# Performance work log

Hardware: AMD Instinct MI355X
Metric: run time of the kernel (lower is better)

## Reference

```python
import jax, jax.numpy as jnp
import numpy as np

B, H, W, C, NH, WS, NB = 8, 64, 64, 384, 12, 8, 2
N = H * W
NWT = WS * WS  # tokens per window
SHIFT = WS // 2

def _rel_index(ws):
    coords = np.stack(np.meshgrid(np.arange(ws), np.arange(ws), indexing='ij')).reshape(2, -1)
    rel = (coords[:, :, None] - coords[:, None, :]).transpose(1, 2, 0)
    rel[..., 0] += ws - 1
    rel[..., 1] += ws - 1
    rel[..., 0] *= 2 * ws - 1
    return rel.sum(-1)  # (ws*ws, ws*ws)

REL_IDX = _rel_index(WS)

def _shift_mask(h, w, ws, shift):
    img = np.zeros((h, w))
    cnt = 0
    for hs in (slice(0, -ws), slice(-ws, -shift), slice(-shift, None)):
        for wsl in (slice(0, -ws), slice(-ws, -shift), slice(-shift, None)):
            img[hs, wsl] = cnt
            cnt += 1
    win = img.reshape(h // ws, ws, w // ws, ws).transpose(0, 2, 1, 3).reshape(-1, ws * ws)
    diff = win[:, None, :] - win[:, :, None]
    return np.where(diff != 0, -100.0, 0.0).astype(np.float32)  # (nW, NWT, NWT)

MASK = jnp.asarray(_shift_mask(H, W, WS, SHIFT))

def _ln(x, g, b, eps=1e-5):
    m = jnp.mean(x, -1, keepdims=True)
    v = jnp.mean((x - m) ** 2, -1, keepdims=True)
    return (x - m) * jax.lax.rsqrt(v + eps) * g + b

def _partition(x):
    b = x.shape[0]
    x = x.reshape(b, H // WS, WS, W // WS, WS, C).transpose(0, 1, 3, 2, 4, 5)
    return x.reshape(-1, NWT, C)

def _reverse(wx, b):
    x = wx.reshape(b, H // WS, W // WS, WS, WS, C).transpose(0, 1, 3, 2, 4, 5)
    return x.reshape(b, H, W, C)

def _attention(xw, qkv_w, qkv_b, proj_w, proj_b, rpb, mask):
    B_, Nt, Cc = xw.shape
    hd = Cc // NH
    qkv = (xw @ qkv_w + qkv_b).reshape(B_, Nt, 3, NH, hd).transpose(2, 0, 3, 1, 4)
    q, k, v = qkv[0], qkv[1], qkv[2]
    bias = rpb[REL_IDX].transpose(2, 0, 1)[None]  # (1, NH, Nt, Nt)
    attn = jnp.einsum('bhnd,bhmd->bhnm', q * (hd ** -0.5), k) + bias
    if mask is not None:
        nW = mask.shape[0]
        attn = attn.reshape(B_ // nW, nW, NH, Nt, Nt) + mask[None, :, None]
        attn = attn.reshape(B_, NH, Nt, Nt)
    attn = jax.nn.softmax(attn, axis=-1)
    out = jnp.einsum('bhnm,bhmd->bhnd', attn, v).transpose(0, 2, 1, 3).reshape(B_, Nt, Cc)
    return out @ proj_w + proj_b

def _swin_block(x, p, shift):
    n1g, n1b, n2g, n2b, qw, qb, pw, pb, w1, b1, w2, b2, rpb = p
    shortcut = x
    h = _ln(x, n1g, n1b)
    if shift > 0:
        h = jnp.roll(h, (-shift, -shift), axis=(1, 2))
    hw = _attention(_partition(h), qw, qb, pw, pb, rpb, MASK if shift > 0 else None)
    h = _reverse(hw, x.shape[0])
    if shift > 0:
        h = jnp.roll(h, (shift, shift), axis=(1, 2))
    x = shortcut + h
    h = _ln(x, n2g, n2b)
    h = jax.nn.gelu(h @ w1 + b1) @ w2 + b2
    return x + h


def setup_inputs() -> dict:
    key = jax.random.key(0)
    ks = jax.random.split(key, 6)
    s = 0.02
    return {
        'x': jax.random.normal(ks[0], (B, N, C), jnp.float32),
        'outer_g': jnp.ones((NB, C), jnp.float32),
        'outer_b': jnp.zeros((NB, C), jnp.float32),
        'n1_g': jnp.ones((NB, C), jnp.float32),
        'n1_b': jnp.zeros((NB, C), jnp.float32),
        'n2_g': jnp.ones((NB, C), jnp.float32),
        'n2_b': jnp.zeros((NB, C), jnp.float32),
        'qkv_w': jax.random.normal(ks[1], (NB, C, 3 * C), jnp.float32) * s,
        'qkv_b': jnp.zeros((NB, 3 * C), jnp.float32),
        'proj_w': jax.random.normal(ks[2], (NB, C, C), jnp.float32) * s,
        'proj_b': jnp.zeros((NB, C), jnp.float32),
        'mlp_w1': jax.random.normal(ks[3], (NB, C, 4 * C), jnp.float32) * s,
        'mlp_b1': jnp.zeros((NB, 4 * C), jnp.float32),
        'mlp_w2': jax.random.normal(ks[4], (NB, 4 * C, C), jnp.float32) * s,
        'mlp_b2': jnp.zeros((NB, C), jnp.float32),
        'rpb': jax.random.normal(ks[5], (NB, (2 * WS - 1) ** 2, NH), jnp.float32) * s,
    }


def reference(x, outer_g, outer_b, n1_g, n1_b, n2_g, n2_b, qkv_w, qkv_b, proj_w, proj_b, mlp_w1, mlp_b1, mlp_w2, mlp_b2, rpb):
    xv = x.reshape(B, H, W, C)
    for i in range(NB):
        shift = 0 if i % 2 == 0 else SHIFT
        p = (n1_g[i], n1_b[i], n2_g[i], n2_b[i], qkv_w[i], qkv_b[i], proj_w[i], proj_b[i],
             mlp_w1[i], mlp_b1[i], mlp_w2[i], mlp_b2[i], rpb[i])
        residual = xv
        xv = _swin_block(_ln(xv, outer_g[i], outer_b[i]), p, shift) + residual
    return xv.reshape(B, N, C)
```

## Files before the change

kernel.cpp:

```cpp
#include <hip/hip_runtime.h>
#include <hip/hip_bf16.h>

#define BATCH 8
#define HDIM 64
#define WDIM 64
#define CC 384
#define NHE 12
#define HD 32
#define NTOK 32768
#define NBLK 2

typedef short short8 __attribute__((ext_vector_type(8)));
typedef float f32x4 __attribute__((ext_vector_type(4)));

__device__ __forceinline__ float bf2f(unsigned short u) {
  return __uint_as_float(((unsigned int)u) << 16);
}
__device__ __forceinline__ unsigned short f2bf(float f) {
  __hip_bfloat16 h = __float2bfloat16(f);
  return *reinterpret_cast<unsigned short*>(&h);
}
__device__ __forceinline__ float wave_sum(float s) {
#pragma unroll
  for (int o = 32; o; o >>= 1) s += __shfl_xor(s, o, 64);
  return s;
}
__device__ __forceinline__ float gelu_f(float x) {
  float y = 0.7978845608028654f * (x + 0.044715f * x * x * x);
  float t = 1.0f - 2.0f / (__expf(2.0f * y) + 1.0f);
  return 0.5f * x * (1.0f + t);
}
__device__ __forceinline__ int regid(int x) {
  return x < 56 ? 0 : (x < 60 ? 1 : 2);
}
__device__ __forceinline__ void gload16(const void* g, void* l) {
  __builtin_amdgcn_global_load_lds(
      (const __attribute__((address_space(1))) unsigned int*)g,
      (__attribute__((address_space(3))) unsigned int*)l, 16, 0, 0);
}

__global__ __launch_bounds__(256) void wconv_kernel(
    const float* __restrict__ src, unsigned short* __restrict__ dst, int K, int N) {
  __shared__ float tile[64 * 65];
  const int bn = blockIdx.x * 64, bk = blockIdx.y * 64;
  const int t = threadIdx.x;
  const int lk = t >> 2, ln = (t & 3) * 16;
  const float* ps = src + (size_t)(bk + lk) * N + bn + ln;
#pragma unroll
  for (int j = 0; j < 4; ++j)
    *(float4*)&tile[lk * 65 + ln + 4 * j] = *(const float4*)(ps + 4 * j);
  __syncthreads();
  const int on = t >> 2, ok = (t & 3) * 16;
  unsigned short ob[16];
#pragma unroll
  for (int j = 0; j < 16; ++j) ob[j] = f2bf(tile[(ok + j) * 65 + on]);
  uint4* pd = (uint4*)(dst + (size_t)(bn + on) * K + bk + ok);
  pd[0] = ((const uint4*)ob)[0];
  pd[1] = ((const uint4*)ob)[1];
}

__global__ __launch_bounds__(256) void bias_prep_kernel(
    const float* __restrict__ rpb, float* __restrict__ biasT) {
  int idx = blockIdx.x * 256 + threadIdx.x;
  int m = idx & 63;
  int n = (idx >> 6) & 63;
  int h = idx >> 12;
  int dr = (n >> 3) - (m >> 3) + 7;
  int dc = (n & 7) - (m & 7) + 7;
  biasT[idx] = rpb[(dr * 15 + dc) * NHE + h];
}

__global__ __launch_bounds__(256) void ln_fused_kernel(
    const float* __restrict__ xin, const float* __restrict__ og,
    const float* __restrict__ ob, const float* __restrict__ n1g,
    const float* __restrict__ n1b, unsigned short* __restrict__ y0h,
    unsigned short* __restrict__ abuf, int shift) {
  const int lane = threadIdx.x & 63;
  const int token = blockIdx.x * 4 + (threadIdx.x >> 6);
  const float* px = xin + (size_t)token * CC;
  float v[6];
#pragma unroll
  for (int j = 0; j < 6; ++j) v[j] = px[j * 64 + lane];
  float s = 0.f;
#pragma unroll
  for (int j = 0; j < 6; ++j) s += v[j];
  s = wave_sum(s);
  float mean = s * (1.0f / CC);
  float q = 0.f;
#pragma unroll
  for (int j = 0; j < 6; ++j) { float d = v[j] - mean; q += d * d; }
  q = wave_sum(q);
  float rstd = rsqrtf(q * (1.0f / CC) + 1e-5f);
  unsigned short* py = y0h + (size_t)token * CC;
#pragma unroll
  for (int j = 0; j < 6; ++j) {
    int d = j * 64 + lane;
    float y = (v[j] - mean) * rstd * og[d] + ob[d];
    py[d] = f2bf(y);
    v[j] = y;
  }
  s = 0.f;
#pragma unroll
  for (int j = 0; j < 6; ++j) s += v[j];
  s = wave_sum(s);
  float mean2 = s * (1.0f / CC);
  q = 0.f;
#pragma unroll
  for (int j = 0; j < 6; ++j) { float d = v[j] - mean2; q += d * d; }
  q = wave_sum(q);
  float rstd2 = rsqrtf(q * (1.0f / CC) + 1e-5f);
  int b = token >> 12;
  int hh = (token >> 6) & 63;
  int ww = token & 63;
  int r = (hh - shift) & 63;
  int c = (ww - shift) & 63;
  int wrow = (((b << 6) + ((r >> 3) << 3) + (c >> 3)) << 6) + ((r & 7) << 3) + (c & 7);
  unsigned short* pa = abuf + (size_t)wrow * CC;
#pragma unroll
  for (int j = 0; j < 6; ++j) {
    int d = j * 64 + lane;
    pa[d] = f2bf((v[j] - mean2) * rstd2 * n1g[d] + n1b[d]);
  }
}

__global__ __launch_bounds__(256, 1) void apl_kernel(
    const unsigned short* __restrict__ qkv, const float* __restrict__ biasT,
    const unsigned short* __restrict__ y0h, const unsigned short* __restrict__ Btp,
    const float* __restrict__ pb, const float* __restrict__ g2,
    const float* __restrict__ b2, unsigned short* __restrict__ x1h,
    unsigned short* __restrict__ abuf, int shift) {
  __shared__ __align__(1024) char smem[65536];
  const int tid = threadIdx.x;
  const int wv = tid >> 6;
  const int lane = tid & 63;
  const int l0 = lane & 15;
  const int q = lane >> 4;
  const int wi = blockIdx.x;
  const int use_mask = (shift != 0);

  unsigned short* P16 = (unsigned short*)(smem + wv * 12288);
  unsigned short* Vt16 = (unsigned short*)(smem + wv * 12288 + 8192);
  float* Ol = (float*)(smem + wv * 12288);
  unsigned short* Obuf = (unsigned short*)(smem + 49152);

  f32x4 pacc[4][6] = {};

  for (int p = 0; p < 3; ++p) {
    const int h = 4 * p + wv;
    const unsigned short* qbase = qkv + (size_t)(wi * 64) * 1152 + h * HD;
    short8 kf[4], qf[4];
#pragma unroll
    for (int mt = 0; mt < 4; ++mt)
      kf[mt] = *(const short8*)(qbase + (size_t)(16 * mt + l0) * 1152 + CC + 8 * q);
#pragma unroll
    for (int nt = 0; nt < 4; ++nt)
      qf[nt] = *(const short8*)(qbase + (size_t)(16 * nt + l0) * 1152 + 8 * q);

    f32x4 acc[4][4];
    const float* bh = biasT + h * 4096;
#pragma unroll
    for (int mt = 0; mt < 4; ++mt)
#pragma unroll
      for (int nt = 0; nt < 4; ++nt)
        acc[mt][nt] = *(const f32x4*)(bh + (l0 + 16 * nt) * 64 + 16 * mt + 4 * q);

    {
      unsigned short varr[32];
      const uint4* pv = (const uint4*)(qbase + (size_t)lane * 1152 + 2 * CC);
      uint4* t4 = (uint4*)varr;
      t4[0] = pv[0]; t4[1] = pv[1]; t4[2] = pv[2]; t4[3] = pv[3];
#pragma unroll
      for (int d = 0; d < 32; ++d)
        Vt16[d * 64 + 8 * ((lane >> 3) ^ (d & 7)) + (lane & 7)] = varr[d];
    }

#pragma unroll
    for (int mt = 0; mt < 4; ++mt)
#pragma unroll
      for (int nt = 0; nt < 4; ++nt)
        acc[mt][nt] = __builtin_amdgcn_mfma_f32_16x16x32_bf16(kf[mt], qf[nt], acc[mt][nt], 0, 0, 0);

    if (use_mask) {
      int wloc = wi & 63;
      int wy = (wloc >> 3) * 8, wx = (wloc & 7) * 8;
      int idn[4], idm[16];
#pragma unroll
      for (int nt = 0; nt < 4; ++nt) {
        int n = l0 + 16 * nt;
        idn[nt] = regid(wy + (n >> 3)) * 3 + regid(wx + (n & 7));
      }
#pragma unroll
      for (int mt = 0; mt < 4; ++mt)
#pragma unroll
        for (int r = 0; r < 4; ++r) {
          int m = 16 * mt + 4 * q + r;
          idm[mt * 4 + r] = regid(wy + (m >> 3)) * 3 + regid(wx + (m & 7));
        }
#pragma unroll
      for (int mt = 0; mt < 4; ++mt)
#pragma unroll
        for (int nt = 0; nt < 4; ++nt)
#pragma unroll
          for (int r = 0; r < 4; ++r)
            acc[mt][nt][r] += (idm[mt * 4 + r] == idn[nt]) ? 0.0f : -100.0f;
    }

    float inv[4];
#pragma unroll
    for (int nt = 0; nt < 4; ++nt) {
      float m0 = -1e30f;
#pragma unroll
      for (int mt = 0; mt < 4; ++mt)
#pragma unroll
        for (int r = 0; r < 4; ++r) m0 = fmaxf(m0, acc[mt][nt][r]);
      m0 = fmaxf(m0, __shfl_xor(m0, 16, 64));
      m0 = fmaxf(m0, __shfl_xor(m0, 32, 64));
      float s0 = 0.f;
#pragma unroll
      for (int mt = 0; mt < 4; ++mt)
#pragma unroll
        for (int r = 0; r < 4; ++r) {
          float e = __expf(acc[mt][nt][r] - m0);
          acc[mt][nt][r] = e;
          s0 += e;
        }
      s0 += __shfl_xor(s0, 16, 64);
      s0 += __shfl_xor(s0, 32, 64);
      inv[nt] = 1.0f / s0;
    }

#pragma unroll
    for (int mt = 0; mt < 4; ++mt)
#pragma unroll
      for (int nt = 0; nt < 4; ++nt) {
        unsigned int lo = (unsigned int)f2bf(acc[mt][nt][0] * inv[nt]) |
                          ((unsigned int)f2bf(acc[mt][nt][1] * inv[nt]) << 16);
        unsigned int hi = (unsigned int)f2bf(acc[mt][nt][2] * inv[nt]) |
                          ((unsigned int)f2bf(acc[mt][nt][3] * inv[nt]) << 16);
        unsigned int* dst = (unsigned int*)&P16[(l0 + 16 * nt) * 64 +
                                                8 * ((2 * mt + (q >> 1)) ^ (l0 & 7)) + 4 * (q & 1)];
        dst[0] = lo;
        dst[1] = hi;
      }
    __syncthreads();

    f32x4 oacc[4][2] = {};
#pragma unroll
    for (int kt = 0; kt < 2; ++kt) {
      short8 pa[4], vb[2];
#pragma unroll
      for (int nt = 0; nt < 4; ++nt)
        pa[nt] = *(const short8*)&P16[(l0 + 16 * nt) * 64 + 8 * ((q + 4 * kt) ^ (l0 & 7))];
#pragma unroll
      for (int dt = 0; dt < 2; ++dt)
        vb[dt] = *(const short8*)&Vt16[(l0 + 16 * dt) * 64 + 8 * ((q + 4 * kt) ^ (l0 & 7))];
#pragma unroll
      for (int nt = 0; nt < 4; ++nt)
#pragma unroll
        for (int dt = 0; dt < 2; ++dt)
          oacc[nt][dt] = __builtin_amdgcn_mfma_f32_16x16x32_bf16(pa[nt], vb[dt], oacc[nt][dt], 0, 0, 0);
    }
    __syncthreads();

#pragma unroll
    for (int nt = 0; nt < 4; ++nt)
#pragma unroll
      for (int dt = 0; dt < 2; ++dt)
#pragma unroll
        for (int r = 0; r < 4; ++r)
          Ol[(16 * nt + 4 * q + r) * 34 + l0 + 16 * dt] = oacc[nt][dt][r];
    __syncthreads();

#pragma unroll
    for (int jj = 0; jj < 4; ++jj) {
      int c = 4 * wv + jj;
      int pos = (c & 8) | ((c ^ lane) & 7);
      unsigned short tmp[8];
#pragma unroll
      for (int e = 0; e < 8; ++e) tmp[e] = f2bf(Ol[lane * 34 + jj * 8 + e]);
      *(uint4*)&Obuf[lane * 128 + pos * 8] = *(const uint4*)tmp;
    }
    __syncthreads();

#pragma unroll
    for (int kfl = 0; kfl < 4; ++kfl) {
      short8 a[4], b[6];
      int c2 = kfl * 4 + q;
      int pos2 = (c2 & 8) | ((c2 ^ l0) & 7);
#pragma unroll
      for (int mt = 0; mt < 4; ++mt)
        a[mt] = *(const short8*)&Obuf[(16 * mt + l0) * 128 + pos2 * 8];
#pragma unroll
      for (int nt = 0; nt < 6; ++nt)
        b[nt] = *(const short8*)(Btp + (size_t)(wv * 96 + nt * 16 + l0) * 384 +
                                 128 * p + 32 * kfl + 8 * q);
#pragma unroll
      for (int mt = 0; mt < 4; ++mt)
#pragma unroll
        for (int nt = 0; nt < 6; ++nt)
          pacc[mt][nt] = __builtin_amdgcn_mfma_f32_16x16x32_bf16(a[mt], b[nt], pacc[mt][nt], 0, 0, 0);
    }
    __syncthreads();
  }

  float pbv[6], g2v[6], b2v[6];
#pragma unroll
  for (int nt = 0; nt < 6; ++nt) {
    int col = wv * 96 + nt * 16 + l0;
    pbv[nt] = pb[col];
    g2v[nt] = g2[col];
    b2v[nt] = b2[col];
  }
  int dstrow[4][4];
#pragma unroll
  for (int mt = 0; mt < 4; ++mt)
#pragma unroll
    for (int rr = 0; rr < 4; ++rr) {
      int m = 16 * mt + 4 * q + rr;
      int grow = wi * 64 + m;
      int b_ = grow >> 12;
      int wl = (grow >> 6) & 63;
      int t = grow & 63;
      int rs = ((wl >> 3) << 3) + (t >> 3);
      int cs = ((wl & 7) << 3) + (t & 7);
      int hh = (rs + shift) & 63;
      int ww = (cs + shift) & 63;
      dstrow[mt][rr] = (((b_ << 6) + hh) << 6) + ww;
    }
#pragma unroll
  for (int mt = 0; mt < 4; ++mt)
#pragma unroll
    for (int nt = 0; nt < 6; ++nt)
#pragma unroll
      for (int rr = 0; rr < 4; ++rr) {
        size_t dst = (size_t)dstrow[mt][rr] * CC + wv * 96 + nt * 16 + l0;
        pacc[mt][nt][rr] += pbv[nt] + bf2f(y0h[dst]);
      }
  float* part = (float*)(smem + 49152);
  float* stats = (float*)(smem + 49152 + 2048);
#pragma unroll
  for (int mt = 0; mt < 4; ++mt)
#pragma unroll
    for (int rr = 0; rr < 4; ++rr) {
      float s = 0.f, ss = 0.f;
#pragma unroll
      for (int nt = 0; nt < 6; ++nt) {
        float v = pacc[mt][nt][rr];
        s += v;
        ss += v * v;
      }
#pragma unroll
      for (int o = 8; o; o >>= 1) {
        s += __shfl_xor(s, o, 64);
        ss += __shfl_xor(ss, o, 64);
      }
      if (l0 == 0) {
        int m = 16 * mt + 4 * q + rr;
        part[(m * 4 + wv) * 2] = s;
        part[(m * 4 + wv) * 2 + 1] = ss;
      }
    }
  __syncthreads();
  if (tid < 64) {
    float s = 0.f, ss = 0.f;
#pragma unroll
    for (int w = 0; w < 4; ++w) {
      s += part[(tid * 4 + w) * 2];
      ss += part[(tid * 4 + w) * 2 + 1];
    }
    float mean = s * (1.0f / CC);
    float var = ss * (1.0f / CC) - mean * mean;
    stats[tid * 2] = mean;
    stats[tid * 2 + 1] = rsqrtf(var + 1e-5f);
  }
  __syncthreads();
#pragma unroll
  for (int mt = 0; mt < 4; ++mt)
#pragma unroll
    for (int rr = 0; rr < 4; ++rr) {
      int m = 16 * mt + 4 * q + rr;
      float mean = stats[m * 2];
      float rstd = stats[m * 2 + 1];
#pragma unroll
      for (int nt = 0; nt < 6; ++nt) {
        float v = pacc[mt][nt][rr];
        size_t dst = (size_t)dstrow[mt][rr] * CC + wv * 96 + nt * 16 + l0;
        x1h[dst] = f2bf(v);
        abuf[dst] = f2bf((v - mean) * rstd * g2v[nt] + b2v[nt]);
      }
    }
}

template <int EPI, int NN, int KK>
__global__ __launch_bounds__(256, 2) void gemm_kernel(
    const unsigned short* __restrict__ A, const unsigned short* __restrict__ Bt,
    const float* __restrict__ bias, float* __restrict__ outf,
    unsigned short* __restrict__ outb, const unsigned short* __restrict__ add0h,
    const float* __restrict__ add1f) {
  __shared__ __align__(1024) char smem[32768];
  unsigned short* As = (unsigned short*)smem;
  unsigned short* Bs = (unsigned short*)(smem + 16384);
  const int tid = threadIdx.x;
  const int lane = tid & 63;
  const int wv = tid >> 6;
  const int wm = wv & 1, wn = wv >> 1;
  const int rowBase = blockIdx.y * 128;
  const int colBase = blockIdx.x * 128;
  const int srow = lane >> 3;
  const int schunk = (lane & 7) ^ srow;
  const unsigned short* pA = A + (size_t)(rowBase + srow) * KK + 8 * schunk;
  const unsigned short* pB = Bt + (size_t)(colBase + srow) * KK + 8 * schunk;
  const int l0 = lane & 15;
  const int q = lane >> 4;
  f32x4 acc[4][4] = {};

  for (int k0 = 0; k0 < KK; k0 += 64) {
    __syncthreads();
#pragma unroll
    for (int i = 0; i < 4; ++i) {
      int c = i * 4 + wv;
      gload16(pA + (size_t)(8 * c) * KK + k0, (char*)As + c * 1024);
      gload16(pB + (size_t)(8 * c) * KK + k0, (char*)Bs + c * 1024);
    }
    __syncthreads();
#pragma unroll
    for (int ksub = 0; ksub < 2; ++ksub) {
      const int sc = ksub * 4 + q;
      short8 af[4], bfr[4];
#pragma unroll
      for (int im = 0; im < 4; ++im) {
        int r = wm * 64 + im * 16 + l0;
        af[im] = *(const short8*)&As[r * 64 + 8 * (sc ^ (r & 7))];
      }
#pragma unroll
      for (int in_ = 0; in_ < 4; ++in_) {
        int r = wn * 64 + in_ * 16 + l0;
        bfr[in_] = *(const short8*)&Bs[r * 64 + 8 * (sc ^ (r & 7))];
      }
#pragma unroll
      for (int im = 0; im < 4; ++im)
#pragma unroll
        for (int in_ = 0; in_ < 4; ++in_)
          acc[im][in_] = __builtin_amdgcn_mfma_f32_16x16x32_bf16(
              af[im], bfr[in_], acc[im][in_], 0, 0, 0);
    }
  }
  const int quad = lane >> 4;
  const int lc = lane & 15;
#pragma unroll
  for (int im = 0; im < 4; ++im) {
    int rb = rowBase + wm * 64 + im * 16 + quad * 4;
#pragma unroll
    for (int in_ = 0; in_ < 4; ++in_) {
      int gcol = colBase + wn * 64 + in_ * 16 + lc;
      float bv = bias[gcol];
#pragma unroll
      for (int r = 0; r < 4; ++r) {
        int grow = rb + r;
        float v = acc[im][in_][r] + bv;
        if (EPI == 0) {
          if (gcol < CC) v *= 0.17677669529663687f;
          outb[(size_t)grow * NN + gcol] = f2bf(v);
        } else if (EPI == 1) {
          outb[(size_t)grow * NN + gcol] = f2bf(gelu_f(v));
        } else {
          size_t dst = (size_t)grow * CC + gcol;
          outf[dst] = bf2f(add0h[dst]) + add1f[dst] + v;
        }
      }
    }
  }
}

extern "C" void kernel_launch(void* const* d_in, const int* in_sizes, int n_in,
                              void* d_out, int out_size, void* d_ws, size_t ws_size,
                              hipStream_t stream) {
  const float* x    = (const float*)d_in[0];
  const float* og   = (const float*)d_in[1];
  const float* ob   = (const float*)d_in[2];
  const float* n1g  = (const float*)d_in[3];
  const float* n1b  = (const float*)d_in[4];
  const float* n2g  = (const float*)d_in[5];
  const float* n2b  = (const float*)d_in[6];
  const float* qkvw = (const float*)d_in[7];
  const float* qkvb = (const float*)d_in[8];
  const float* pw   = (const float*)d_in[9];
  const float* pb   = (const float*)d_in[10];
  const float* w1   = (const float*)d_in[11];
  const float* b1   = (const float*)d_in[12];
  const float* w2   = (const float*)d_in[13];
  const float* b2   = (const float*)d_in[14];
  const float* rpb  = (const float*)d_in[15];
  float* out = (float*)d_out;

  char* ws = (char*)d_ws;
  unsigned short* y0h   = (unsigned short*)(ws);
  unsigned short* x1h   = (unsigned short*)(ws + 25165824);
  unsigned short* a_bf  = (unsigned short*)(ws + 50331648);
  unsigned short* big_bf= (unsigned short*)(ws + 100663296);
  unsigned short* wt    = (unsigned short*)(ws + 201326592);
  float* biasT          = (float*)(ws + 100663296 + 75497472);

  for (int i = 0; i < NBLK; ++i) {
    unsigned short* wq = wt + (size_t)i * 1769472;
    wconv_kernel<<<dim3(18, 6), 256, 0, stream>>>(qkvw + (size_t)i * 442368, wq, 384, 1152);
    wconv_kernel<<<dim3(6, 6), 256, 0, stream>>>(pw + (size_t)i * 147456, wq + 442368, 384, 384);
    wconv_kernel<<<dim3(24, 6), 256, 0, stream>>>(w1 + (size_t)i * 589824, wq + 589824, 384, 1536);
    wconv_kernel<<<dim3(6, 24), 256, 0, stream>>>(w2 + (size_t)i * 589824, wq + 1179648, 1536, 384);
  }

  for (int i = 0; i < NBLK; ++i) {
    const float* xin = (i == 0) ? x : out;
    int shift = (i & 1) ? 4 : 0;
    unsigned short* wq = wt + (size_t)i * 1769472;
    ln_fused_kernel<<<8192, 256, 0, stream>>>(xin, og + i * 384, ob + i * 384,
                                              n1g + i * 384, n1b + i * 384, y0h, a_bf, shift);
    gemm_kernel<0, 1152, 384><<<dim3(9, 256), 256, 0, stream>>>(
        a_bf, wq, qkvb + i * 1152, nullptr, big_bf, nullptr, nullptr);
    bias_prep_kernel<<<192, 256, 0, stream>>>(rpb + i * 2700, biasT);
    apl_kernel<<<512, 256, 0, stream>>>(big_bf, biasT, y0h, wq + 442368,
                                        pb + i * 384, n2g + i * 384, n2b + i * 384,
                                        x1h, a_bf, shift);
    gemm_kernel<1, 1536, 384><<<dim3(12, 256), 256, 0, stream>>>(
        a_bf, wq + 589824, b1 + i * 1536, nullptr, big_bf, nullptr, nullptr);
    gemm_kernel<3, 384, 1536><<<dim3(3, 256), 256, 0, stream>>>(
        big_bf, wq + 1179648, b2 + i * 384, out, nullptr, x1h, xin);
  }
}
```

Before: 708.6 us.

## Prefetch next head's QKV in attention kernel and relax block barriers

Loads the next head's K/Q/V fragments into registers while the current head is processed, which hides global load latency. Most block-wide __syncthreads calls are replaced with per-wave LDS waitcnt fences, since each wave owns its own P/V/O scratch region. MFMA sections are wrapped in s_setprio, and launch bounds are raised to 2 blocks per CU. The extra prefetch registers may raise register pressure, and the higher occupancy target could cause spills. The 64KB of shared memory per block may also stop a second block from fitting on a CU.

```diff
diff --git a/kernel.cpp b/kernel.cpp
--- a/kernel.cpp
+++ b/kernel.cpp
@@ -123,7 +123,7 @@
   }
 }
 
-__global__ __launch_bounds__(256, 1) void apl_kernel(
+__global__ __launch_bounds__(256, 2) void apl_kernel(
     const unsigned short* __restrict__ qkv, const float* __restrict__ biasT,
     const unsigned short* __restrict__ y0h, const unsigned short* __restrict__ Btp,
     const float* __restrict__ pb, const float* __restrict__ g2,
@@ -144,17 +144,34 @@
   unsigned short* Obuf = (unsigned short*)(smem + 49152);
 
   f32x4 pacc[4][6] = {};
-
+  const unsigned short* qkw = qkv + (size_t)(wi * 64) * 1152;
+
+#define LOADP(PP, KD, QD, VD)                                                        \
+  {                                                                                  \
+    const unsigned short* qb_ = qkw + (4 * (PP) + wv) * HD;                          \
+    const uint4* pv_ = (const uint4*)(qb_ + (size_t)lane * 1152 + 2 * CC);           \
+    VD[0] = pv_[0]; VD[1] = pv_[1]; VD[2] = pv_[2]; VD[3] = pv_[3];                  \
+    _Pragma("unroll") for (int mt_ = 0; mt_ < 4; ++mt_)                              \
+        KD[mt_] = *(const short8*)(qb_ + (size_t)(16 * mt_ + l0) * 1152 + CC + 8 * q); \
+    _Pragma("unroll") for (int nt_ = 0; nt_ < 4; ++nt_)                              \
+        QD[nt_] = *(const short8*)(qb_ + (size_t)(16 * nt_ + l0) * 1152 + 8 * q);    \
+  }
+#define LDS_FENCE() asm volatile("s_waitcnt lgkmcnt(0)" ::: "memory")
+
+  short8 kf[4], qf[4];
+  uint4 varr4[4];
+  LOADP(0, kf, qf, varr4);
+
+#pragma unroll
   for (int p = 0; p < 3; ++p) {
     const int h = 4 * p + wv;
-    const unsigned short* qbase = qkv + (size_t)(wi * 64) * 1152 + h * HD;
-    short8 kf[4], qf[4];
-#pragma unroll
-    for (int mt = 0; mt < 4; ++mt)
-      kf[mt] = *(const short8*)(qbase + (size_t)(16 * mt + l0) * 1152 + CC + 8 * q);
-#pragma unroll
-    for (int nt = 0; nt < 4; ++nt)
-      qf[nt] = *(const short8*)(qbase + (size_t)(16 * nt + l0) * 1152 + 8 * q);
+
+    {
+      const unsigned short* varr = (const unsigned short*)varr4;
+#pragma unroll
+      for (int d = 0; d < 32; ++d)
+        Vt16[d * 64 + 8 * ((lane >> 3) ^ (d & 7)) + (lane & 7)] = varr[d];
+    }
 
     f32x4 acc[4][4];
     const float* bh = biasT + h * 4096;
@@ -164,21 +181,17 @@
       for (int nt = 0; nt < 4; ++nt)
         acc[mt][nt] = *(const f32x4*)(bh + (l0 + 16 * nt) * 64 + 16 * mt + 4 * q);
 
-    {
-      unsigned short varr[32];
-      const uint4* pv = (const uint4*)(qbase + (size_t)lane * 1152 + 2 * CC);
-      uint4* t4 = (uint4*)varr;
-      t4[0] = pv[0]; t4[1] = pv[1]; t4[2] = pv[2]; t4[3] = pv[3];
-#pragma unroll
-      for (int d = 0; d < 32; ++d)
-        Vt16[d * 64 + 8 * ((lane >> 3) ^ (d & 7)) + (lane & 7)] = varr[d];
-    }
-
+    short8 kfn[4], qfn[4];
+    uint4 varrn[4];
+    if (p < 2) { LOADP(p + 1, kfn, qfn, varrn); }
+
+    __builtin_amdgcn_s_setprio(1);
 #pragma unroll
     for (int mt = 0; mt < 4; ++mt)
 #pragma unroll
       for (int nt = 0; nt < 4; ++nt)
         acc[mt][nt] = __builtin_amdgcn_mfma_f32_16x16x32_bf16(kf[mt], qf[nt], acc[mt][nt], 0, 0, 0);
+    __builtin_amdgcn_s_setprio(0);
 
     if (use_mask) {
       int wloc = wi & 63;
@@ -242,9 +255,10 @@
         dst[0] = lo;
         dst[1] = hi;
       }
-    __syncthreads();
+    LDS_FENCE();
 
     f32x4 oacc[4][2] = {};
+    __builtin_amdgcn_s_setprio(1);
 #pragma unroll
     for (int kt = 0; kt < 2; ++kt) {
       short8 pa[4], vb[2];
@@ -260,7 +274,8 @@
         for (int dt = 0; dt < 2; ++dt)
           oacc[nt][dt] = __builtin_amdgcn_mfma_f32_16x16x32_bf16(pa[nt], vb[dt], oacc[nt][dt], 0, 0, 0);
     }
-    __syncthreads();
+    __builtin_amdgcn_s_setprio(0);
+    LDS_FENCE();
 
 #pragma unroll
     for (int nt = 0; nt < 4; ++nt)
@@ -269,17 +284,23 @@
 #pragma unroll
         for (int r = 0; r < 4; ++r)
           Ol[(16 * nt + 4 * q + r) * 34 + l0 + 16 * dt] = oacc[nt][dt][r];
-    __syncthreads();
-
+    LDS_FENCE();
+
+    uint4 opack[4];
+    int posv[4];
 #pragma unroll
     for (int jj = 0; jj < 4; ++jj) {
       int c = 4 * wv + jj;
-      int pos = (c & 8) | ((c ^ lane) & 7);
+      posv[jj] = (c & 8) | ((c ^ lane) & 7);
       unsigned short tmp[8];
 #pragma unroll
       for (int e = 0; e < 8; ++e) tmp[e] = f2bf(Ol[lane * 34 + jj * 8 + e]);
-      *(uint4*)&Obuf[lane * 128 + pos * 8] = *(const uint4*)tmp;
-    }
+      opack[jj] = *(const uint4*)tmp;
+    }
+    __syncthreads();
+#pragma unroll
+    for (int jj = 0; jj < 4; ++jj)
+      *(uint4*)&Obuf[lane * 128 + posv[jj] * 8] = opack[jj];
     __syncthreads();
 
 #pragma unroll
@@ -294,14 +315,25 @@
       for (int nt = 0; nt < 6; ++nt)
         b[nt] = *(const short8*)(Btp + (size_t)(wv * 96 + nt * 16 + l0) * 384 +
                                  128 * p + 32 * kfl + 8 * q);
+      __builtin_amdgcn_s_setprio(1);
 #pragma unroll
       for (int mt = 0; mt < 4; ++mt)
 #pragma unroll
         for (int nt = 0; nt < 6; ++nt)
           pacc[mt][nt] = __builtin_amdgcn_mfma_f32_16x16x32_bf16(a[mt], b[nt], pacc[mt][nt], 0, 0, 0);
-    }
-    __syncthreads();
-  }
+      __builtin_amdgcn_s_setprio(0);
+    }
+
+    if (p < 2) {
+#pragma unroll
+      for (int j = 0; j < 4; ++j) {
+        kf[j] = kfn[j];
+        qf[j] = qfn[j];
+        varr4[j] = varrn[j];
+      }
+    }
+  }
+  __syncthreads();
 
   float pbv[6], g2v[6], b2v[6];
 #pragma unroll
@@ -389,6 +421,8 @@
         abuf[dst] = f2bf((v - mean) * rstd * g2v[nt] + b2v[nt]);
       }
     }
+#undef LOADP
+#undef LDS_FENCE
 }
 
 template <int EPI, int NN, int KK>
```

Result: no change. 702.2 us (-0.9%).

## Double-buffer GEMM LDS loads, relax attention barriers, and raise MFMA priority

Applied to the files above, without the earlier changes.

The GEMM kernel now prefetches the next K tile into a second LDS buffer, with vmcnt waits and raw barriers, so global loads overlap the MFMA work on the current tile. LDS use doubles to 64KB, which may limit occupancy under launch_bounds(256,2). In the attention kernel, block-wide __syncthreads on per-wave private LDS regions are replaced with lgkmcnt fences, leaving only the barriers around the shared Obuf. s_setprio is raised around MFMA sections to favour compute issue.

```diff
diff --git a/kernel.cpp b/kernel.cpp
--- a/kernel.cpp
+++ b/kernel.cpp
@@ -143,6 +143,8 @@
   float* Ol = (float*)(smem + wv * 12288);
   unsigned short* Obuf = (unsigned short*)(smem + 49152);
 
+#define LDS_FENCE() asm volatile("s_waitcnt lgkmcnt(0)" ::: "memory")
+
   f32x4 pacc[4][6] = {};
 
   for (int p = 0; p < 3; ++p) {
@@ -174,11 +176,13 @@
         Vt16[d * 64 + 8 * ((lane >> 3) ^ (d & 7)) + (lane & 7)] = varr[d];
     }
 
+    __builtin_amdgcn_s_setprio(1);
 #pragma unroll
     for (int mt = 0; mt < 4; ++mt)
 #pragma unroll
       for (int nt = 0; nt < 4; ++nt)
         acc[mt][nt] = __builtin_amdgcn_mfma_f32_16x16x32_bf16(kf[mt], qf[nt], acc[mt][nt], 0, 0, 0);
+    __builtin_amdgcn_s_setprio(0);
 
     if (use_mask) {
       int wloc = wi & 63;
@@ -242,9 +246,10 @@
         dst[0] = lo;
         dst[1] = hi;
       }
-    __syncthreads();
+    LDS_FENCE();
 
     f32x4 oacc[4][2] = {};
+    __builtin_amdgcn_s_setprio(1);
 #pragma unroll
     for (int kt = 0; kt < 2; ++kt) {
       short8 pa[4], vb[2];
@@ -260,7 +265,8 @@
         for (int dt = 0; dt < 2; ++dt)
           oacc[nt][dt] = __builtin_amdgcn_mfma_f32_16x16x32_bf16(pa[nt], vb[dt], oacc[nt][dt], 0, 0, 0);
     }
-    __syncthreads();
+    __builtin_amdgcn_s_setprio(0);
+    LDS_FENCE();
 
 #pragma unroll
     for (int nt = 0; nt < 4; ++nt)
@@ -269,17 +275,23 @@
 #pragma unroll
         for (int r = 0; r < 4; ++r)
           Ol[(16 * nt + 4 * q + r) * 34 + l0 + 16 * dt] = oacc[nt][dt][r];
-    __syncthreads();
-
+    LDS_FENCE();
+
+    uint4 opack[4];
+    int posv[4];
 #pragma unroll
     for (int jj = 0; jj < 4; ++jj) {
       int c = 4 * wv + jj;
-      int pos = (c & 8) | ((c ^ lane) & 7);
+      posv[jj] = (c & 8) | ((c ^ lane) & 7);
       unsigned short tmp[8];
 #pragma unroll
       for (int e = 0; e < 8; ++e) tmp[e] = f2bf(Ol[lane * 34 + jj * 8 + e]);
-      *(uint4*)&Obuf[lane * 128 + pos * 8] = *(const uint4*)tmp;
-    }
+      opack[jj] = *(const uint4*)tmp;
+    }
+    __syncthreads();
+#pragma unroll
+    for (int jj = 0; jj < 4; ++jj)
+      *(uint4*)&Obuf[lane * 128 + posv[jj] * 8] = opack[jj];
     __syncthreads();
 
 #pragma unroll
@@ -294,14 +306,16 @@
       for (int nt = 0; nt < 6; ++nt)
         b[nt] = *(const short8*)(Btp + (size_t)(wv * 96 + nt * 16 + l0) * 384 +
                                  128 * p + 32 * kfl + 8 * q);
+      __builtin_amdgcn_s_setprio(1);
 #pragma unroll
       for (int mt = 0; mt < 4; ++mt)
 #pragma unroll
         for (int nt = 0; nt < 6; ++nt)
           pacc[mt][nt] = __builtin_amdgcn_mfma_f32_16x16x32_bf16(a[mt], b[nt], pacc[mt][nt], 0, 0, 0);
-    }
-    __syncthreads();
-  }
+      __builtin_amdgcn_s_setprio(0);
+    }
+  }
+  __syncthreads();
 
   float pbv[6], g2v[6], b2v[6];
 #pragma unroll
@@ -389,6 +403,7 @@
         abuf[dst] = f2bf((v - mean) * rstd * g2v[nt] + b2v[nt]);
       }
     }
+#undef LDS_FENCE
 }
 
 template <int EPI, int NN, int KK>
@@ -397,9 +412,7 @@
     const float* __restrict__ bias, float* __restrict__ outf,
     unsigned short* __restrict__ outb, const unsigned short* __restrict__ add0h,
     const float* __restrict__ add1f) {
-  __shared__ __align__(1024) char smem[32768];
-  unsigned short* As = (unsigned short*)smem;
-  unsigned short* Bs = (unsigned short*)(smem + 16384);
+  __shared__ __align__(1024) char smem[65536];
   const int tid = threadIdx.x;
   const int lane = tid & 63;
   const int wv = tid >> 6;
@@ -414,15 +427,32 @@
   const int q = lane >> 4;
   f32x4 acc[4][4] = {};
 
+#pragma unroll
+  for (int i = 0; i < 4; ++i) {
+    int c = i * 4 + wv;
+    gload16(pA + (size_t)(8 * c) * KK, smem + c * 1024);
+    gload16(pB + (size_t)(8 * c) * KK, smem + 16384 + c * 1024);
+  }
+
+#pragma unroll 2
   for (int k0 = 0; k0 < KK; k0 += 64) {
-    __syncthreads();
-#pragma unroll
-    for (int i = 0; i < 4; ++i) {
-      int c = i * 4 + wv;
-      gload16(pA + (size_t)(8 * c) * KK + k0, (char*)As + c * 1024);
-      gload16(pB + (size_t)(8 * c) * KK + k0, (char*)Bs + c * 1024);
-    }
-    __syncthreads();
+    const int cur = (k0 >> 6) & 1;
+    char* curb = smem + cur * 32768;
+    if (k0 + 64 < KK) {
+      char* nxtb = smem + (cur ^ 1) * 32768;
+#pragma unroll
+      for (int i = 0; i < 4; ++i) {
+        int c = i * 4 + wv;
+        gload16(pA + (size_t)(8 * c) * KK + k0 + 64, nxtb + c * 1024);
+        gload16(pB + (size_t)(8 * c) * KK + k0 + 64, nxtb + 16384 + c * 1024);
+      }
+      asm volatile("s_waitcnt vmcnt(8)" ::: "memory");
+    } else {
+      asm volatile("s_waitcnt vmcnt(0)" ::: "memory");
+    }
+    __builtin_amdgcn_s_barrier();
+    const unsigned short* As = (const unsigned short*)curb;
+    const unsigned short* Bs = (const unsigned short*)(curb + 16384);
 #pragma unroll
     for (int ksub = 0; ksub < 2; ++ksub) {
       const int sc = ksub * 4 + q;
@@ -437,13 +467,16 @@
         int r = wn * 64 + in_ * 16 + l0;
         bfr[in_] = *(const short8*)&Bs[r * 64 + 8 * (sc ^ (r & 7))];
       }
+      __builtin_amdgcn_s_setprio(1);
 #pragma unroll
       for (int im = 0; im < 4; ++im)
 #pragma unroll
         for (int in_ = 0; in_ < 4; ++in_)
           acc[im][in_] = __builtin_amdgcn_mfma_f32_16x16x32_bf16(
               af[im], bfr[in_], acc[im][in_], 0, 0, 0);
-    }
+      __builtin_amdgcn_s_setprio(0);
+    }
+    __builtin_amdgcn_s_barrier();
   }
   const int quad = lane >> 4;
   const int lc = lane & 15;
```

Result: no change. 704.8 us (-0.5%).
